# Optimization experiments

Hardware: AMD Instinct MI355X
Metric: run time of the kernel (lower is better)

Reference implementation:

```python
import jax, jax.numpy as jnp
import numpy as np

B, H, S, D = 2, 32, 16384, 64


def setup_inputs() -> dict:
    key = jax.random.key(0)
    kq, kk, kv = jax.random.split(key, 3)
    return {
        "query_states": jax.random.normal(kq, (B, H, S, D), dtype=jnp.float32),
        "key_states": jax.random.normal(kk, (B, H, S, D), dtype=jnp.float32),
        "value_states": jax.random.normal(kv, (B, H, S, D), dtype=jnp.float32),
    }


def reference(query_states, key_states, value_states):
    # Feature map: elu(x) + 1 (strictly positive kernel features)
    k_feat = jax.nn.elu(key_states) + 1.0          # [B,H,S,Dk]
    q_feat = jax.nn.elu(query_states) + 1.0        # [B,H,S,Dk]

    # Compressive memory: sum over sequence of k^T v outer products -> [B,H,Dk,Dv]
    memory = jnp.einsum("bhsk,bhsv->bhkv", k_feat, value_states)
    # Normalization: sum of key features over sequence -> [B,H,Dk]
    normalization = jnp.sum(k_feat, axis=2)

    # Retrieval: q @ memory, normalized by q . normalization
    retrieved = jnp.einsum("bhsk,bhkv->bhsv", q_feat, memory)   # [B,H,S,Dv]
    denominator = jnp.einsum("bhsk,bhk->bhs", q_feat, normalization)
    return retrieved / denominator[..., None]
```

## Files before the change

kernel.cpp:

```cpp
#include <hip/hip_runtime.h>
#include <math.h>

#define BH_ 64
#define S_ 16384
#define D_ 64
#define LD_ 68
#define P1_CHUNKS 16
#define P1_ROWS (S_ / P1_CHUNKS)
#define P2_CHUNKS 32
#define P2_ROWS (S_ / P2_CHUNKS)

__device__ __forceinline__ float elu1(float x) {
    return x > 0.0f ? x + 1.0f : __expf(x);
}

#define FMA4(s, m, a) { (a).x += (s) * (m).x; (a).y += (s) * (m).y; (a).z += (s) * (m).z; (a).w += (s) * (m).w; }

__global__ __launch_bounds__(256) void p1_kernel(const float* __restrict__ K,
                                                 const float* __restrict__ V,
                                                 float* __restrict__ Mg,
                                                 float* __restrict__ zg) {
    __shared__ float kf[64 * LD_];
    __shared__ float vf[64 * LD_];
    __shared__ float zpart[4][64];

    const int tid = threadIdx.x;
    const int bh = blockIdx.y;
    const int chunk = blockIdx.x;
    const int ki = tid >> 4;
    const int vj = tid & 15;
    const int zd = tid & 63;
    const int zq = tid >> 6;

    const size_t base = ((size_t)bh * S_ + (size_t)chunk * P1_ROWS) * D_;
    const float* Kb = K + base;
    const float* Vb = V + base;

    float4 acc0 = {0.f,0.f,0.f,0.f}, acc1 = acc0, acc2 = acc0, acc3 = acc0;
    float zacc = 0.f;

    for (int s0 = 0; s0 < P1_ROWS; s0 += 64) {
        __syncthreads();
        #pragma unroll
        for (int k = 0; k < 4; ++k) {
            const int row = k * 16 + (tid >> 4);
            const int col = (tid & 15) * 4;
            float4 kv = *(const float4*)(Kb + (size_t)(s0 + row) * D_ + col);
            float4 vv = *(const float4*)(Vb + (size_t)(s0 + row) * D_ + col);
            float4 kx;
            kx.x = elu1(kv.x); kx.y = elu1(kv.y); kx.z = elu1(kv.z); kx.w = elu1(kv.w);
            *(float4*)&kf[row * LD_ + col] = kx;
            *(float4*)&vf[row * LD_ + col] = vv;
        }
        __syncthreads();

        #pragma unroll
        for (int j = 0; j < 16; ++j)
            zacc += kf[(zq * 16 + j) * LD_ + zd];

        #pragma unroll 4
        for (int s = 0; s < 64; ++s) {
            float4 a = *(const float4*)&kf[s * LD_ + 4 * ki];
            float4 b = *(const float4*)&vf[s * LD_ + 4 * vj];
            FMA4(a.x, b, acc0);
            FMA4(a.y, b, acc1);
            FMA4(a.z, b, acc2);
            FMA4(a.w, b, acc3);
        }
    }

    zpart[zq][zd] = zacc;
    __syncthreads();
    if (tid < 64) {
        float z = zpart[0][tid] + zpart[1][tid] + zpart[2][tid] + zpart[3][tid];
        atomicAdd(&zg[bh * 64 + tid], z);
    }

    float* Mb = Mg + (size_t)bh * 4096 + (size_t)(4 * ki) * 64 + 4 * vj;
    atomicAdd(&Mb[0 * 64 + 0], acc0.x); atomicAdd(&Mb[0 * 64 + 1], acc0.y);
    atomicAdd(&Mb[0 * 64 + 2], acc0.z); atomicAdd(&Mb[0 * 64 + 3], acc0.w);
    atomicAdd(&Mb[1 * 64 + 0], acc1.x); atomicAdd(&Mb[1 * 64 + 1], acc1.y);
    atomicAdd(&Mb[1 * 64 + 2], acc1.z); atomicAdd(&Mb[1 * 64 + 3], acc1.w);
    atomicAdd(&Mb[2 * 64 + 0], acc2.x); atomicAdd(&Mb[2 * 64 + 1], acc2.y);
    atomicAdd(&Mb[2 * 64 + 2], acc2.z); atomicAdd(&Mb[2 * 64 + 3], acc2.w);
    atomicAdd(&Mb[3 * 64 + 0], acc3.x); atomicAdd(&Mb[3 * 64 + 1], acc3.y);
    atomicAdd(&Mb[3 * 64 + 2], acc3.z); atomicAdd(&Mb[3 * 64 + 3], acc3.w);
}

__global__ __launch_bounds__(256) void p2_kernel(const float* __restrict__ Q,
                                                 const float* __restrict__ Mg,
                                                 const float* __restrict__ zg,
                                                 float* __restrict__ Ob) {
    __shared__ float Ms[64 * 64];
    __shared__ float qs[64 * LD_];
    __shared__ float zs[64];

    const int tid = threadIdx.x;
    const int bh = blockIdx.y;
    const int chunk = blockIdx.x;
    const int si = tid >> 4;
    const int vj = tid & 15;
    const int lane = tid & 63;

    #pragma unroll
    for (int k = 0; k < 4; ++k)
        *(float4*)&Ms[k * 1024 + tid * 4] =
            *(const float4*)&Mg[(size_t)bh * 4096 + k * 1024 + tid * 4];
    if (tid < 16)
        *(float4*)&zs[tid * 4] = *(const float4*)&zg[bh * 64 + tid * 4];

    const size_t base = ((size_t)bh * S_ + (size_t)chunk * P2_ROWS) * D_;
    const float* Qb = Q + base;
    float* Outb = Ob + base;

    const int drow = (tid >> 6) * 16 + (lane >> 2);
    const int seg = lane & 3;

    for (int s0 = 0; s0 < P2_ROWS; s0 += 64) {
        __syncthreads();
        #pragma unroll
        for (int k = 0; k < 4; ++k) {
            const int row = k * 16 + (tid >> 4);
            const int col = (tid & 15) * 4;
            float4 qv = *(const float4*)(Qb + (size_t)(s0 + row) * D_ + col);
            float4 qx;
            qx.x = elu1(qv.x); qx.y = elu1(qv.y); qx.z = elu1(qv.z); qx.w = elu1(qv.w);
            *(float4*)&qs[row * LD_ + col] = qx;
        }
        __syncthreads();

        float dsum = 0.f;
        #pragma unroll
        for (int j = 0; j < 4; ++j) {
            float4 qq = *(const float4*)&qs[drow * LD_ + seg * 16 + j * 4];
            float4 zz = *(const float4*)&zs[seg * 16 + j * 4];
            dsum += qq.x * zz.x + qq.y * zz.y + qq.z * zz.z + qq.w * zz.w;
        }
        dsum += __shfl_xor(dsum, 1);
        dsum += __shfl_xor(dsum, 2);
        const float dinv = 1.0f / dsum;

        float4 a0 = {0.f,0.f,0.f,0.f}, a1 = a0, a2 = a0, a3 = a0;
        #pragma unroll 2
        for (int dk = 0; dk < 64; dk += 4) {
            float4 m0 = *(const float4*)&Ms[(dk + 0) * 64 + 4 * vj];
            float4 m1 = *(const float4*)&Ms[(dk + 1) * 64 + 4 * vj];
            float4 m2 = *(const float4*)&Ms[(dk + 2) * 64 + 4 * vj];
            float4 m3 = *(const float4*)&Ms[(dk + 3) * 64 + 4 * vj];
            float4 q0 = *(const float4*)&qs[(4 * si + 0) * LD_ + dk];
            float4 q1 = *(const float4*)&qs[(4 * si + 1) * LD_ + dk];
            float4 q2 = *(const float4*)&qs[(4 * si + 2) * LD_ + dk];
            float4 q3 = *(const float4*)&qs[(4 * si + 3) * LD_ + dk];
            FMA4(q0.x, m0, a0); FMA4(q0.y, m1, a0); FMA4(q0.z, m2, a0); FMA4(q0.w, m3, a0);
            FMA4(q1.x, m0, a1); FMA4(q1.y, m1, a1); FMA4(q1.z, m2, a1); FMA4(q1.w, m3, a1);
            FMA4(q2.x, m0, a2); FMA4(q2.y, m1, a2); FMA4(q2.z, m2, a2); FMA4(q2.w, m3, a2);
            FMA4(q3.x, m0, a3); FMA4(q3.y, m1, a3); FMA4(q3.z, m2, a3); FMA4(q3.w, m3, a3);
        }

        #pragma unroll
        for (int r = 0; r < 4; ++r) {
            const float dv_ = __shfl(dinv, 16 * (si & 3) + 4 * r);
            float4 o = (r == 0) ? a0 : (r == 1) ? a1 : (r == 2) ? a2 : a3;
            o.x *= dv_; o.y *= dv_; o.z *= dv_; o.w *= dv_;
            *(float4*)(Outb + (size_t)(s0 + 4 * si + r) * D_ + 4 * vj) = o;
        }
    }
}

extern "C" void kernel_launch(void* const* d_in, const int* in_sizes, int n_in,
                              void* d_out, int out_size, void* d_ws, size_t ws_size,
                              hipStream_t stream) {
    const float* Q = (const float*)d_in[0];
    const float* K = (const float*)d_in[1];
    const float* V = (const float*)d_in[2];
    float* out = (float*)d_out;

    float* Mg = (float*)d_ws;
    float* zg = Mg + (size_t)BH_ * 4096;
    const size_t init_bytes = ((size_t)BH_ * 4096 + (size_t)BH_ * 64) * sizeof(float);

    hipMemsetAsync(d_ws, 0, init_bytes, stream);

    dim3 blk(256);
    dim3 g1(P1_CHUNKS, BH_);
    p1_kernel<<<g1, blk, 0, stream>>>(K, V, Mg, zg);

    dim3 g2(P2_CHUNKS, BH_);
    p2_kernel<<<g2, blk, 0, stream>>>(Q, Mg, zg, out);
}
```

Measured before the change: 824.1 us.

## Double-buffer p1 K/V staging with direct-to-LDS V loads and per-wave accumulation

Rewrites the K^T V reduction kernel. The 64-row tile becomes 32-row stages with V double-buffered through global_load_lds and the next K stage prefetched into registers. Each wave now owns an 8-row slice and computes a full 64x64 partial with 8x8 outputs per thread, and the waves are summed through LDS before one set of atomics. The aim is to overlap global loads with FMA work and raise register-level reuse, at the cost of a serialized cross-wave LDS reduction and higher register pressure.

```diff
diff --git a/kernel.cpp b/kernel.cpp
--- a/kernel.cpp
+++ b/kernel.cpp
@@ -5,8 +5,10 @@
 #define S_ 16384
 #define D_ 64
 #define LD_ 68
+#define KLD 68
 #define P1_CHUNKS 16
 #define P1_ROWS (S_ / P1_CHUNKS)
+#define P1_STAGE 32
 #define P2_CHUNKS 32
 #define P2_ROWS (S_ / P2_CHUNKS)
 
@@ -15,76 +17,148 @@
 }
 
 #define FMA4(s, m, a) { (a).x += (s) * (m).x; (a).y += (s) * (m).y; (a).z += (s) * (m).z; (a).w += (s) * (m).w; }
-
-__global__ __launch_bounds__(256) void p1_kernel(const float* __restrict__ K,
-                                                 const float* __restrict__ V,
-                                                 float* __restrict__ Mg,
-                                                 float* __restrict__ zg) {
-    __shared__ float kf[64 * LD_];
-    __shared__ float vf[64 * LD_];
+#define ADD4(a, b)    { (a).x += (b).x; (a).y += (b).y; (a).z += (b).z; (a).w += (b).w; }
+
+__device__ __forceinline__ void load_lds_16B(const float* g, float* l) {
+    __builtin_amdgcn_global_load_lds(
+        (const __attribute__((address_space(1))) unsigned int*)g,
+        (__attribute__((address_space(3))) unsigned int*)l, 16, 0, 0);
+}
+
+__global__ __launch_bounds__(256, 4) void p1_kernel(const float* __restrict__ K,
+                                                    const float* __restrict__ V,
+                                                    float* __restrict__ Mg,
+                                                    float* __restrict__ zg) {
+    __shared__ float kf[P1_STAGE * KLD];
+    __shared__ float vf[2][P1_STAGE * D_];
     __shared__ float zpart[4][64];
 
-    const int tid = threadIdx.x;
-    const int bh = blockIdx.y;
+    const int tid  = threadIdx.x;
+    const int wid  = tid >> 6;
+    const int lane = tid & 63;
+    const int ki   = lane >> 3;
+    const int vj   = lane & 7;
+
+    const int bh    = blockIdx.y;
     const int chunk = blockIdx.x;
-    const int ki = tid >> 4;
-    const int vj = tid & 15;
-    const int zd = tid & 63;
-    const int zq = tid >> 6;
-
     const size_t base = ((size_t)bh * S_ + (size_t)chunk * P1_ROWS) * D_;
     const float* Kb = K + base;
     const float* Vb = V + base;
 
-    float4 acc0 = {0.f,0.f,0.f,0.f}, acc1 = acc0, acc2 = acc0, acc3 = acc0;
+    float4 acc[8][2];
+    #pragma unroll
+    for (int a = 0; a < 8; ++a) {
+        acc[a][0] = make_float4(0.f, 0.f, 0.f, 0.f);
+        acc[a][1] = make_float4(0.f, 0.f, 0.f, 0.f);
+    }
     float zacc = 0.f;
 
-    for (int s0 = 0; s0 < P1_ROWS; s0 += 64) {
-        __syncthreads();
-        #pragma unroll
-        for (int k = 0; k < 4; ++k) {
-            const int row = k * 16 + (tid >> 4);
-            const int col = (tid & 15) * 4;
-            float4 kv = *(const float4*)(Kb + (size_t)(s0 + row) * D_ + col);
-            float4 vv = *(const float4*)(Vb + (size_t)(s0 + row) * D_ + col);
-            float4 kx;
-            kx.x = elu1(kv.x); kx.y = elu1(kv.y); kx.z = elu1(kv.z); kx.w = elu1(kv.w);
-            *(float4*)&kf[row * LD_ + col] = kx;
-            *(float4*)&vf[row * LD_ + col] = vv;
-        }
-        __syncthreads();
-
-        #pragma unroll
-        for (int j = 0; j < 16; ++j)
-            zacc += kf[(zq * 16 + j) * LD_ + zd];
-
+    const int nstage = P1_ROWS / P1_STAGE;
+
+    {
+        float4 k0 = *(const float4*)(Kb + tid * 4);
+        float4 k1 = *(const float4*)(Kb + 1024 + tid * 4);
+        float* vdst = &vf[0][wid * 512];
+        load_lds_16B(Vb + wid * 512 + lane * 4, vdst);
+        load_lds_16B(Vb + wid * 512 + 256 + lane * 4, vdst + 256);
+        float4 e0, e1;
+        e0.x = elu1(k0.x); e0.y = elu1(k0.y); e0.z = elu1(k0.z); e0.w = elu1(k0.w);
+        e1.x = elu1(k1.x); e1.y = elu1(k1.y); e1.z = elu1(k1.z); e1.w = elu1(k1.w);
+        *(float4*)&kf[(tid >> 4) * KLD + 4 * (tid & 15)] = e0;
+        *(float4*)&kf[(16 + (tid >> 4)) * KLD + 4 * (tid & 15)] = e1;
+        __syncthreads();
+    }
+
+    int buf = 0;
+    for (int t = 0; t < nstage; ++t) {
+        const int nt = t + 1;
+        float4 nk0, nk1;
+        if (nt < nstage) {
+            const float* Ks = Kb + (size_t)nt * P1_STAGE * D_;
+            const float* Vs = Vb + (size_t)nt * P1_STAGE * D_;
+            nk0 = *(const float4*)(Ks + tid * 4);
+            nk1 = *(const float4*)(Ks + 1024 + tid * 4);
+            float* vdst = &vf[buf ^ 1][wid * 512];
+            load_lds_16B(Vs + wid * 512 + lane * 4, vdst);
+            load_lds_16B(Vs + wid * 512 + 256 + lane * 4, vdst + 256);
+        }
+
+        const float* kfw = &kf[(8 * wid) * KLD];
+        #pragma unroll
+        for (int j = 0; j < 8; ++j)
+            zacc += kfw[j * KLD + lane];
+
+        const float* vfw = &vf[buf][(8 * wid) * D_];
         #pragma unroll 4
-        for (int s = 0; s < 64; ++s) {
-            float4 a = *(const float4*)&kf[s * LD_ + 4 * ki];
-            float4 b = *(const float4*)&vf[s * LD_ + 4 * vj];
-            FMA4(a.x, b, acc0);
-            FMA4(a.y, b, acc1);
-            FMA4(a.z, b, acc2);
-            FMA4(a.w, b, acc3);
-        }
-    }
-
-    zpart[zq][zd] = zacc;
+        for (int s = 0; s < 8; ++s) {
+            float4 k0 = *(const float4*)&kfw[s * KLD + 8 * ki];
+            float4 k1 = *(const float4*)&kfw[s * KLD + 8 * ki + 4];
+            float4 v0 = *(const float4*)&vfw[s * D_ + 8 * vj];
+            float4 v1 = *(const float4*)&vfw[s * D_ + 8 * vj + 4];
+            FMA4(k0.x, v0, acc[0][0]); FMA4(k0.x, v1, acc[0][1]);
+            FMA4(k0.y, v0, acc[1][0]); FMA4(k0.y, v1, acc[1][1]);
+            FMA4(k0.z, v0, acc[2][0]); FMA4(k0.z, v1, acc[2][1]);
+            FMA4(k0.w, v0, acc[3][0]); FMA4(k0.w, v1, acc[3][1]);
+            FMA4(k1.x, v0, acc[4][0]); FMA4(k1.x, v1, acc[4][1]);
+            FMA4(k1.y, v0, acc[5][0]); FMA4(k1.y, v1, acc[5][1]);
+            FMA4(k1.z, v0, acc[6][0]); FMA4(k1.z, v1, acc[6][1]);
+            FMA4(k1.w, v0, acc[7][0]); FMA4(k1.w, v1, acc[7][1]);
+        }
+
+        __syncthreads();
+        if (nt < nstage) {
+            float4 e0, e1;
+            e0.x = elu1(nk0.x); e0.y = elu1(nk0.y); e0.z = elu1(nk0.z); e0.w = elu1(nk0.w);
+            e1.x = elu1(nk1.x); e1.y = elu1(nk1.y); e1.z = elu1(nk1.z); e1.w = elu1(nk1.w);
+            *(float4*)&kf[(tid >> 4) * KLD + 4 * (tid & 15)] = e0;
+            *(float4*)&kf[(16 + (tid >> 4)) * KLD + 4 * (tid & 15)] = e1;
+        }
+        buf ^= 1;
+        __syncthreads();
+    }
+
+    zpart[wid][lane] = zacc;
     __syncthreads();
     if (tid < 64) {
         float z = zpart[0][tid] + zpart[1][tid] + zpart[2][tid] + zpart[3][tid];
         atomicAdd(&zg[bh * 64 + tid], z);
     }
 
-    float* Mb = Mg + (size_t)bh * 4096 + (size_t)(4 * ki) * 64 + 4 * vj;
-    atomicAdd(&Mb[0 * 64 + 0], acc0.x); atomicAdd(&Mb[0 * 64 + 1], acc0.y);
-    atomicAdd(&Mb[0 * 64 + 2], acc0.z); atomicAdd(&Mb[0 * 64 + 3], acc0.w);
-    atomicAdd(&Mb[1 * 64 + 0], acc1.x); atomicAdd(&Mb[1 * 64 + 1], acc1.y);
-    atomicAdd(&Mb[1 * 64 + 2], acc1.z); atomicAdd(&Mb[1 * 64 + 3], acc1.w);
-    atomicAdd(&Mb[2 * 64 + 0], acc2.x); atomicAdd(&Mb[2 * 64 + 1], acc2.y);
-    atomicAdd(&Mb[2 * 64 + 2], acc2.z); atomicAdd(&Mb[2 * 64 + 3], acc2.w);
-    atomicAdd(&Mb[3 * 64 + 0], acc3.x); atomicAdd(&Mb[3 * 64 + 1], acc3.y);
-    atomicAdd(&Mb[3 * 64 + 2], acc3.z); atomicAdd(&Mb[3 * 64 + 3], acc3.w);
+    float4* red = (float4*)&vf[0][0];
+    for (int w = 1; w < 4; ++w) {
+        if (wid == w) {
+            #pragma unroll
+            for (int a = 0; a < 8; ++a) {
+                red[(2 * a + 0) * 64 + lane] = acc[a][0];
+                red[(2 * a + 1) * 64 + lane] = acc[a][1];
+            }
+        }
+        __syncthreads();
+        if (wid == 0) {
+            #pragma unroll
+            for (int a = 0; a < 8; ++a) {
+                float4 r0 = red[(2 * a + 0) * 64 + lane];
+                float4 r1 = red[(2 * a + 1) * 64 + lane];
+                ADD4(acc[a][0], r0);
+                ADD4(acc[a][1], r1);
+            }
+        }
+        __syncthreads();
+    }
+    if (wid == 0) {
+        float* Mb = Mg + (size_t)bh * 4096 + (size_t)(8 * ki) * 64 + 8 * vj;
+        #pragma unroll
+        for (int a = 0; a < 8; ++a) {
+            atomicAdd(&Mb[a * 64 + 0], acc[a][0].x);
+            atomicAdd(&Mb[a * 64 + 1], acc[a][0].y);
+            atomicAdd(&Mb[a * 64 + 2], acc[a][0].z);
+            atomicAdd(&Mb[a * 64 + 3], acc[a][0].w);
+            atomicAdd(&Mb[a * 64 + 4], acc[a][1].x);
+            atomicAdd(&Mb[a * 64 + 5], acc[a][1].y);
+            atomicAdd(&Mb[a * 64 + 6], acc[a][1].z);
+            atomicAdd(&Mb[a * 64 + 7], acc[a][1].w);
+        }
+    }
 }
 
 __global__ __launch_bounds__(256) void p2_kernel(const float* __restrict__ Q,
```

Measured after the change: 897.7 us. +8.9%, slower.
